# Optimization experiments

Hardware: AMD Instinct MI355X
Metric: run time of the kernel (lower is better)

## Reference

```python
import jax, jax.numpy as jnp
import numpy as np

MAX_SPAN_WIDTH = 12
THRESHOLD = 0.5


def _span_table(num_words):
    starts, ends = [], []
    for s in range(num_words):
        for e in range(s, min(num_words, s + MAX_SPAN_WIDTH)):
            starts.append(s)
            ends.append(e)
    return np.asarray(starts, np.int32), np.asarray(ends, np.int32)


def _mlp(x, w1, b1, w2, b2):
    # Linear -> LeakyReLU(0.01) -> Linear
    return jax.nn.leaky_relu(x @ w1 + b1, negative_slope=0.01) @ w2 + b2


def setup_inputs() -> dict:
    B, L, H, E, W, DFF = 8, 1024, 768, 16, 504, 512
    key = jax.random.key(0)
    ks = jax.random.split(key, 9)
    hidden_states = jax.random.normal(ks[0], (B, L, H), dtype=jnp.float32)
    # layout: first E tokens are entity-type tokens, next 2*W tokens are text (2 subwords/word)
    ent_mask = np.zeros((B, L), np.int32); ent_mask[:, :E] = 1
    text_mask = np.zeros((B, L), np.int32); text_mask[:, E:E + 2 * W] = 1
    word_index = np.full((B, L), -1, np.int32)
    word_index[:, E:E + 2 * W] = np.repeat(np.arange(W, dtype=np.int32), 2)[None, :]
    s = 0.02
    return {
        "hidden_states": hidden_states,
        "ent_w1": jax.random.normal(ks[1], (H, DFF), jnp.float32) * s,
        "ent_b1": jnp.zeros((DFF,), jnp.float32),
        "ent_w2": jax.random.normal(ks[2], (DFF, H), jnp.float32) * s,
        "ent_b2": jnp.zeros((H,), jnp.float32),
        "span_w1": jax.random.normal(ks[3], (2 * H, DFF), jnp.float32) * s,
        "span_b1": jnp.zeros((DFF,), jnp.float32),
        "span_w2": jax.random.normal(ks[4], (DFF, H), jnp.float32) * s,
        "span_b2": jnp.zeros((H,), jnp.float32),
        "text_mask": jnp.asarray(text_mask),
        "ent_mask": jnp.asarray(ent_mask),
        "word_index": jnp.asarray(word_index),
        "num_words": W,
        "num_ent": E,
    }


def reference(hidden_states, ent_w1, ent_b1, ent_w2, ent_b2,
              span_w1, span_b1, span_w2, span_b2,
              text_mask, ent_mask, word_index, num_words, num_ent):
    B, L, H = hidden_states.shape
    W, E = int(num_words), int(num_ent)

    # ---- word-level mean pooling over subword tokens (WordTokenRepresentation) ----
    valid = (text_mask == 1) & (word_index >= 0)                       # [B,L]
    oh = ((word_index[..., None] == jnp.arange(W)) & valid[..., None]).astype(hidden_states.dtype)  # [B,L,W]
    counts = jnp.maximum(oh.sum(axis=1), 1.0)                          # [B,W]
    word_emb = jnp.einsum('blw,blh->bwh', oh, hidden_states) / counts[..., None]

    # ---- gather entity-type tokens in order (EntityTokenRepresentation) ----
    keyv = jnp.where(ent_mask == 1, jnp.arange(L), L + jnp.arange(L))
    ent_pos = jnp.argsort(keyv, axis=-1)[:, :E]                        # [B,E]
    ent_tok = jnp.take_along_axis(hidden_states, ent_pos[..., None], axis=1)  # [B,E,H]
    ent_vec = _mlp(ent_tok, ent_w1, ent_b1, ent_w2, ent_b2)            # [B,E,H]

    # ---- span representations (all spans of width < MAX_SPAN_WIDTH) ----
    starts_np, ends_np = _span_table(W)                                # [N]
    span_in = jnp.concatenate([word_emb[:, starts_np], word_emb[:, ends_np]], axis=-1)  # [B,N,2H]
    span_vec = _mlp(span_in, span_w1, span_b1, span_w2, span_b2)       # [B,N,H]

    # ---- matching logits ----
    logits = jnp.einsum('bnh,beh->bne', span_vec, ent_vec)             # [B,N,E]

    # ---- NMS-style greedy decode (flat mode): threshold + score sort + overlap rejection ----
    N = logits.shape[1]
    probs = jax.nn.sigmoid(logits).reshape(B, N * E)
    cstart = jnp.repeat(jnp.asarray(starts_np), E)                     # [N*E]
    cend = jnp.repeat(jnp.asarray(ends_np), E)
    order = jnp.argsort(-probs, axis=-1)                               # score-descending
    probs_s = jnp.take_along_axis(probs, order, axis=-1)
    s_s, e_s = cstart[order], cend[order]
    pos = jnp.arange(W)

    def decode_one(pr, ss, ee):
        def body(cov, x):
            p, s, e = x
            m = (pos >= s) & (pos <= e)                                # candidate span mask over words
            take = (p > THRESHOLD) & ~jnp.any(cov & m)                 # flat: reject any overlap
            return cov | (m & take), take
        _, taken = jax.lax.scan(body, jnp.zeros((W,), bool), (pr, ss, ee))
        return taken

    taken_sorted = jax.vmap(decode_one)(probs_s, s_s, e_s)             # [B,N*E]
    inv = jnp.argsort(order, axis=-1)
    selected = jnp.take_along_axis(taken_sorted, inv, axis=-1).reshape(B, N, E)
    return logits, selected
```

## Files before the change

kernel.cpp:

```cpp
#include <hip/hip_runtime.h>
#include <hip/hip_bf16.h>
#include <stdint.h>

#define B_ 8
#define L_ 1024
#define H_ 768
#define E_ 16
#define W_ 504
#define DFF_ 512
#define N_ 5982
#define NE_ (N_*E_)
#define BNE_ (B_*NE_)
#define MAXK48 0x0000FFFFFFFFFFFFull
#define PT6_ 6

typedef unsigned long long u64;
typedef unsigned int u32;

__device__ __forceinline__ int rowstart_of(int s){
    int s0 = W_ - 11;
    if (s <= s0) return 12*s;
    int t = s - s0;
    return 12*s0 + t*11 - (t*(t-1))/2;
}

__device__ __forceinline__ u64 shflup_u64(u64 x, int d){
    u32 lo = (u32)__shfl_up((int)(u32)x, d, 64);
    u32 hi = (u32)__shfl_up((int)(u32)(x >> 32), d, 64);
    return ((u64)hi << 32) | (u64)lo;
}
__device__ __forceinline__ u64 shflxor_u64(u64 x, int m){
    u32 lo = (u32)__shfl_xor((int)(u32)x, m, 64);
    u32 hi = (u32)__shfl_xor((int)(u32)(x >> 32), m, 64);
    return ((u64)hi << 32) | (u64)lo;
}

__global__ void k_prolog(const int* __restrict__ ent_mask, int* __restrict__ ent_pos,
                         int* __restrict__ starts, int* __restrict__ ends,
                         int* __restrict__ tokc){
    int blk = blockIdx.x; int tid = threadIdx.x;
    if (blk == 8){
        for (int s = tid; s < W_; s += 256){
            int rs = rowstart_of(s);
            int cnt = min(12, W_ - s);
            for (int i = 0; i < cnt; i++){ starts[rs+i] = s; ends[rs+i] = s+i; }
        }
        for (int i = tid; i < B_*W_; i += 256) tokc[i] = 0;
        return;
    }
    __shared__ u32 wt[4]; __shared__ u32 cbase;
    int b = blk;
    int lane = tid & 63, wave = tid >> 6;
    if (tid == 0) cbase = 0;
    __syncthreads();
    for (int base = 0; base < L_; base += 256){
        int l = base + tid;
        bool f = (ent_mask[b*L_ + l] == 1);
        u64 bal = __ballot(f);
        if (lane == 0) wt[wave] = (u32)__popcll(bal);
        __syncthreads();
        u32 pre = cbase;
        for (int w = 0; w < 4; w++) if (w < wave) pre += wt[w];
        if (f){
            u32 rank = pre + (u32)__popcll(bal & ((1ull<<lane)-1ull));
            if (rank < E_) ent_pos[b*E_ + rank] = l;
        }
        __syncthreads();
        if (tid == 0){ u32 r = cbase; for (int w = 0; w < 4; w++) r += wt[w]; cbase = r; }
        __syncthreads();
    }
    u32 totEnt = cbase;
    if (totEnt >= E_) return;
    for (int base = 0; base < L_; base += 256){
        int l = base + tid;
        bool f = (ent_mask[b*L_ + l] != 1);
        u64 bal = __ballot(f);
        if (lane == 0) wt[wave] = (u32)__popcll(bal);
        __syncthreads();
        u32 pre = cbase;
        for (int w = 0; w < 4; w++) if (w < wave) pre += wt[w];
        if (f){
            u32 rank = pre + (u32)__popcll(bal & ((1ull<<lane)-1ull));
            if (rank < E_) ent_pos[b*E_ + rank] = l;
        }
        __syncthreads();
        if (tid == 0){ u32 r = cbase; for (int w = 0; w < 4; w++) r += wt[w]; cbase = r; }
        __syncthreads();
    }
}

__global__ void k_toklist(const int* __restrict__ tm, const int* __restrict__ wi,
                          int* __restrict__ tok, int* __restrict__ tokc){
    int i = blockIdx.x*256 + threadIdx.x;
    if (i >= B_*L_) return;
    int w = wi[i];
    if (tm[i] == 1 && w >= 0 && w < W_){
        int b = i / L_;
        int bw = b*W_ + w;
        int pos = atomicAdd(&tokc[bw], 1);
        if (pos < 4) tok[bw*4 + pos] = i - b*L_;
    }
}

__global__ void k_poolsort(const float* __restrict__ hs, const int* __restrict__ tok,
                           const int* __restrict__ tokc, float* __restrict__ wemb){
    __shared__ int stok[4]; __shared__ int scnt;
    int bw = blockIdx.x;
    int b = bw / W_;
    int tid = threadIdx.x;
    if (tid == 0){
        int c = tokc[bw]; int cc = min(c, 4);
        int v[4];
        for (int k = 0; k < cc; k++) v[k] = tok[bw*4 + k];
        for (int a = 1; a < cc; a++){ int x = v[a]; int j = a-1; while (j >= 0 && v[j] > x){ v[j+1] = v[j]; j--; } v[j+1] = x; }
        for (int k = 0; k < cc; k++) stok[k] = v[k];
        scnt = c;
    }
    __syncthreads();
    int c = scnt; int cc = min(c, 4);
    float denom = (float)max(c, 1);
    for (int h = tid; h < H_; h += 256){
        double s = 0.0;
        for (int k = 0; k < cc; k++)
            s += (double)hs[((size_t)(b*L_ + stok[k]))*H_ + h];
        wemb[(size_t)bw*H_ + h] = (float)(s / (double)denom);
    }
}

__global__ void k_ent1(const float* __restrict__ hs, const int* __restrict__ ent_pos,
                       const float* __restrict__ w1, const float* __restrict__ b1,
                       float* __restrict__ hidg){
    __shared__ float x[H_];
    int blk = blockIdx.x;
    int be = blk >> 1; int half = blk & 1;
    int b = be >> 4;
    int tid = threadIdx.x;
    int pos = ent_pos[be];
    const float* xp = hs + ((size_t)b*L_ + pos)*H_;
    for (int j = tid; j < H_; j += 256) x[j] = xp[j];
    __syncthreads();
    int d = half*256 + tid;
    float a0=0.f,a1=0.f,a2=0.f,a3=0.f;
    const float* wp = w1 + d;
    #pragma unroll 8
    for (int h = 0; h < H_; h += 4){
        a0 += x[h+0]*wp[(size_t)(h+0)*DFF_];
        a1 += x[h+1]*wp[(size_t)(h+1)*DFF_];
        a2 += x[h+2]*wp[(size_t)(h+2)*DFF_];
        a3 += x[h+3]*wp[(size_t)(h+3)*DFF_];
    }
    float acc = ((a0+a1)+(a2+a3)) + b1[d];
    hidg[(size_t)be*DFF_ + d] = acc > 0.f ? acc : 0.01f*acc;
}

__global__ void k_ent2(const float* __restrict__ hidg,
                       const float* __restrict__ w2, const float* __restrict__ b2,
                       float* __restrict__ ent_vec){
    __shared__ float hsd[DFF_];
    int blk = blockIdx.x;
    int be = blk / 3; int third = blk % 3;
    int tid = threadIdx.x;
    const float* hp = hidg + (size_t)be*DFF_;
    for (int j = tid; j < DFF_; j += 256) hsd[j] = hp[j];
    __syncthreads();
    int j = third*256 + tid;
    float a0=0.f,a1=0.f,a2=0.f,a3=0.f;
    const float* wp = w2 + j;
    #pragma unroll 8
    for (int d = 0; d < DFF_; d += 4){
        a0 += hsd[d+0]*wp[(size_t)(d+0)*H_];
        a1 += hsd[d+1]*wp[(size_t)(d+1)*H_];
        a2 += hsd[d+2]*wp[(size_t)(d+2)*H_];
        a3 += hsd[d+3]*wp[(size_t)(d+3)*H_];
    }
    ent_vec[(size_t)be*H_ + j] = ((a0+a1)+(a2+a3)) + b2[j];
}

__global__ void k_Mc(const float* __restrict__ span_w2, const float* __restrict__ span_b2,
                     const float* __restrict__ ent_vec, float* __restrict__ M,
                     float* __restrict__ cvec){
    int blk = blockIdx.x;
    if (blk == 256){
        int i = threadIdx.x;
        if (i < B_*E_){
            const float* ev = ent_vec + (size_t)i*H_;
            double acc = 0.0;
            for (int h = 0; h < H_; h++) acc += (double)span_b2[h]*(double)ev[h];
            cvec[i] = (float)acc;
        }
        return;
    }
    int b = blk/32; int dbase = (blk%32)*16;
    int tid = threadIdx.x; int d = dbase + (tid>>4); int e = tid&15;
    const float* ev = ent_vec + ((size_t)b*E_ + e)*H_;
    const float* wr = span_w2 + (size_t)d*H_;
    double p0=0.0, p1=0.0;
    for (int h = 0; h < H_; h += 2){
        p0 += (double)wr[h]*(double)ev[h];
        p1 += (double)wr[h+1]*(double)ev[h+1];
    }
    M[((size_t)b*DFF_ + d)*E_ + e] = (float)(p0+p1);
}

__global__ void k_pq(const float* __restrict__ wemb, const float* __restrict__ w1,
                     float* __restrict__ PQ, int b0){
    __shared__ float As[16][68];
    __shared__ float Bs[16][68];
    int bx = blockIdx.x & 15;
    int by = blockIdx.x >> 4;
    int tid = threadIdx.x;
    int tm = tid >> 4, tn = tid & 15;
    const float* A0 = wemb + (size_t)b0*W_*H_;
    int colbase = bx*64;
    const float* Bbase = (colbase < DFF_) ? w1 : (w1 + (size_t)H_*DFF_);
    int bcol0 = (colbase < DFF_) ? colbase : (colbase - DFF_);
    float acc[4][4] = {{0.f}};
    int ar = tid >> 2, akq = tid & 3;
    int bkk = tid >> 4, bcq = tid & 15;
    const int ROWS = 4*W_;
    for (int k0 = 0; k0 < H_; k0 += 16){
        {
            int gr = by*64 + ar;
            float4 av;
            if (gr < ROWS) av = *(const float4*)(A0 + (size_t)gr*H_ + k0 + akq*4);
            else av = make_float4(0.f,0.f,0.f,0.f);
            As[akq*4+0][ar] = av.x; As[akq*4+1][ar] = av.y;
            As[akq*4+2][ar] = av.z; As[akq*4+3][ar] = av.w;
        }
        {
            float4 bv = *(const float4*)(Bbase + (size_t)(k0+bkk)*DFF_ + bcol0 + bcq*4);
            Bs[bkk][bcq*4+0] = bv.x; Bs[bkk][bcq*4+1] = bv.y;
            Bs[bkk][bcq*4+2] = bv.z; Bs[bkk][bcq*4+3] = bv.w;
        }
        __syncthreads();
        #pragma unroll
        for (int kk = 0; kk < 16; kk++){
            float4 a = *(const float4*)&As[kk][tm*4];
            float4 bv = *(const float4*)&Bs[kk][tn*4];
            acc[0][0] += a.x*bv.x; acc[0][1] += a.x*bv.y; acc[0][2] += a.x*bv.z; acc[0][3] += a.x*bv.w;
            acc[1][0] += a.y*bv.x; acc[1][1] += a.y*bv.y; acc[1][2] += a.y*bv.z; acc[1][3] += a.y*bv.w;
            acc[2][0] += a.z*bv.x; acc[2][1] += a.z*bv.y; acc[2][2] += a.z*bv.z; acc[2][3] += a.z*bv.w;
            acc[3][0] += a.w*bv.x; acc[3][1] += a.w*bv.y; acc[3][2] += a.w*bv.z; acc[3][3] += a.w*bv.w;
        }
        __syncthreads();
    }
    #pragma unroll
    for (int r = 0; r < 4; r++){
        int gr = by*64 + tm*4 + r;
        if (gr < ROWS){
            float4 ov = make_float4(acc[r][0], acc[r][1], acc[r][2], acc[r][3]);
            *(float4*)(PQ + (size_t)gr*1024 + colbase + tn*4) = ov;
        }
    }
}

__global__ void k_logits(const float* __restrict__ PQ, const float* __restrict__ Mmat,
                         const float* __restrict__ cvec, const float* __restrict__ span_b1,
                         float* __restrict__ logits, float* __restrict__ outL, int b0){
    __shared__ float Ps[DFF_];
    __shared__ float hid[DFF_];
    __shared__ double redw[64];
    __shared__ float csh[E_];
    int blk = blockIdx.x;
    int bl = blk / W_; int s = blk - bl*W_;
    int b = b0 + bl;
    int tid = threadIdx.x;
    int lane = tid & 63, wave = tid >> 6;
    int ee = tid & 15; int g = tid >> 4;
    float Mreg[32];
    {
        const float* Mp = Mmat + (size_t)b*DFF_*E_ + (size_t)(g*32)*E_ + ee;
        #pragma unroll
        for (int i = 0; i < 32; i++) Mreg[i] = Mp[(size_t)i*E_];
    }
    const float* P = PQ + ((size_t)(bl*W_ + s))*1024;
    for (int d = tid; d < DFF_; d += 256) Ps[d] = P[d] + span_b1[d];
    if (tid < E_) csh[tid] = cvec[b*E_ + tid];
    __syncthreads();
    int nsp = min(12, W_ - s);
    int nbase = rowstart_of(s);
    for (int i = 0; i < nsp; i++){
        int e = s + i;
        const float* Q = PQ + ((size_t)(bl*W_ + e))*1024 + DFF_;
        for (int d = tid; d < DFF_; d += 256){
            float h = Ps[d] + Q[d];
            hid[d] = h > 0.f ? h : 0.01f*h;
        }
        __syncthreads();
        {
            int d0 = g*32;
            double a0=0.0, a1=0.0, a2=0.0, a3=0.0;
            #pragma unroll
            for (int k = 0; k < 32; k += 4){
                a0 += (double)hid[d0+k+0]*(double)Mreg[k+0];
                a1 += (double)hid[d0+k+1]*(double)Mreg[k+1];
                a2 += (double)hid[d0+k+2]*(double)Mreg[k+2];
                a3 += (double)hid[d0+k+3]*(double)Mreg[k+3];
            }
            double acc = (a0+a1)+(a2+a3);
            double t = acc + __shfl_down(acc, 32, 64);
            t = t + __shfl_down(t, 16, 64);
            if (lane < 16) redw[wave*16 + lane] = t;
        }
        __syncthreads();
        if (tid < E_){
            double t = ((redw[tid] + redw[16+tid]) + (redw[32+tid] + redw[48+tid]))
                     + (double)csh[tid];
            float lg = (float)t;
            size_t oi = ((size_t)b*N_ + nbase + i)*E_ + tid;
            logits[oi] = lg;
            outL[oi] = lg;
        }
        __syncthreads();
    }
}

__global__ void k_spanbest(const float* __restrict__ logits,
                           const int* __restrict__ starts, const int* __restrict__ ends,
                           u64* __restrict__ candS, float* __restrict__ outSel){
    int idx = blockIdx.x*256 + threadIdx.x;
    if (idx >= B_*N_) return;
    int b = idx / N_; int n = idx - b*N_;
    const float* lg = logits + (size_t)b*NE_ + (size_t)n*16;
    u64 best = ~0ull;
    for (int e = 0; e < 16; e++){
        float prob = 1.0f/(1.0f + expf(-lg[e]));
        if (prob > 0.5f){
            u32 key24 = (~__float_as_uint(prob)) & 0xFFFFFFu;
            u64 pk = ((u64)key24 << 24) | (u64)(u32)(n*16 + e);
            best = best < pk ? best : pk;
        }
    }
    int s = starts[n], e2 = ends[n];
    int len = e2 - s + 1;
    u64 packed = best;
    if (best != ~0ull)
        packed = best | ((u64)(u32)s << 48) | ((u64)(u32)(len-1) << 57);
    candS[idx] = packed;
    float* selp = outSel + (size_t)BNE_ + (size_t)b*NE_ + (size_t)n*16;
    float4 z = make_float4(0.f,0.f,0.f,0.f);
    *(float4*)(selp+0)  = z; *(float4*)(selp+4)  = z;
    *(float4*)(selp+8)  = z; *(float4*)(selp+12) = z;
}

__device__ __forceinline__ void decode_wave(const u64* sp, int n,
                                            float* __restrict__ outSel, int b){
    int lane = threadIdx.x & 63;
    u64 scov[8];
    #pragma unroll
    for (int k = 0; k < 8; k++) scov[k] = 0ull;
    int covcnt = 0;
    for (int base = 0; base < n; base += 64){
        int i = base + lane;
        bool has = i < n;
        u64 v = has ? sp[i] : ~0ull;
        int s   = (int)((v >> 48) & 0x1FFull);
        int len = (int)((v >> 57) & 0xFull) + 1;
        u32 c   = (u32)(v & 0xFFFFFFull);
        int w0 = s >> 6, sh0 = s & 63;
        int w1i = (w0 < 7) ? w0 + 1 : 7;
        u64 full = (1ull << len) - 1ull;
        u64 m0 = has ? (full << sh0) : 0ull;
        u64 m1 = (has && sh0 + len > 64) ? (full >> (64 - sh0)) : 0ull;
        u64 myc0 = 0ull, myc1 = 0ull;
        #pragma unroll
        for (int k = 0; k < 8; k++){
            if (w0  == k) myc0 = scov[k];
            if (w1i == k) myc1 = scov[k];
        }
        bool alive = has && (((myc0 & m0) | (myc1 & m1)) == 0ull);
        bool accept = false;
        u64 balv = __ballot(alive);
        if (balv){
            u64 pm[8];
            #pragma unroll
            for (int k = 0; k < 8; k++){
                u64 t = 0ull;
                if (alive){
                    if (w0  == k) t |= m0;
                    if (w1i == k) t |= m1;
                }
                pm[k] = t;
            }
            #pragma unroll
            for (int st = 1; st < 64; st <<= 1){
                #pragma unroll
                for (int k = 0; k < 8; k++) pm[k] |= shflup_u64(pm[k], st);
            }
            u64 ex0 = 0ull, ex1 = 0ull;
            #pragma unroll
            for (int k = 0; k < 8; k++){
                u64 e = shflup_u64(pm[k], 1);
                e = (lane == 0) ? 0ull : e;
                if (w0  == k) ex0 = e;
                if (w1i == k) ex1 = e;
            }
            bool blocked = (((ex0 & m0) | (ex1 & m1)) != 0ull);
            bool newacc = alive && !blocked;
            accept = newacc;
            u64 am[8];
            #pragma unroll
            for (int k = 0; k < 8; k++){
                u64 t = 0ull;
                if (newacc){
                    if (w0  == k) t |= m0;
                    if (w1i == k) t |= m1;
                }
                am[k] = t;
            }
            #pragma unroll
            for (int st = 1; st < 64; st <<= 1){
                #pragma unroll
                for (int k = 0; k < 8; k++) am[k] |= shflxor_u64(am[k], st);
            }
            #pragma unroll
            for (int k = 0; k < 8; k++){
                covcnt += (int)__popcll(am[k]);
                scov[k] |= am[k];
            }
            u64 pend = __ballot(alive && blocked);
            u32 vlo = (u32)v, vhi = (u32)(v >> 32);
            u64 accm = 0ull;
            while (pend){
                int j = (int)__builtin_ctzll(pend);
                pend &= pend - 1ull;
#if __has_builtin(__builtin_amdgcn_readlane)
                u32 jlo = (u32)__builtin_amdgcn_readlane((int)vlo, j);
                u32 jhi = (u32)__builtin_amdgcn_readlane((int)vhi, j);
#else
                u32 jlo = (u32)__shfl((int)vlo, j, 64);
                u32 jhi = (u32)__shfl((int)vhi, j, 64);
#endif
                u64 jv = ((u64)jhi << 32) | (u64)jlo;
                int js   = (int)((jv >> 48) & 0x1FFull);
                int jlen = (int)((jv >> 57) & 0xFull) + 1;
                int jw0 = js >> 6, jsh = js & 63;
                int jw1 = (jw0 < 7) ? jw0 + 1 : 7;
                u64 jfull = (1ull << jlen) - 1ull;
                u64 jm0 = jfull << jsh;
                u64 jm1 = (jsh + jlen > 64) ? (jfull >> (64 - jsh)) : 0ull;
                u64 c0 = 0ull, c1 = 0ull;
                #pragma unroll
                for (int k = 0; k < 8; k++){
                    if (jw0 == k) c0 = scov[k];
                    if (jw1 == k) c1 = scov[k];
                }
                bool ok = (((c0 & jm0) | (c1 & jm1)) == 0ull);
                u64 okm = ok ? ~0ull : 0ull;
                #pragma unroll
                for (int k = 0; k < 8; k++){
                    u64 add = 0ull;
                    if (jw0 == k) add |= jm0;
                    if (jw1 == k) add |= jm1;
                    scov[k] |= (add & okm);
                }
                covcnt += ok ? jlen : 0;
                accm |= (okm & (1ull << j));
            }
            if (((accm >> lane) & 1ull) != 0ull) accept = true;
        }
        if (accept)
            outSel[(size_t)BNE_ + (size_t)b*NE_ + (size_t)c] = 1.0f;
        if (covcnt >= W_) break;
    }
}

__global__ __launch_bounds__(1024) void k_tail(const u64* __restrict__ candS,
                                               float* __restrict__ outSel){
    __shared__ u64 cs[6032];
    __shared__ u64 Ma[512], Mb[512];
    __shared__ u32 wtot[16];
    __shared__ int nsh;
    int b = blockIdx.x; int tid = threadIdx.x;
    int lane = tid & 63, wave = tid >> 6;
    const u64* cSg = candS + (size_t)b*N_;

    #pragma unroll
    for (int k = 0; k < 5; k++) cs[tid + k*1024] = cSg[tid + k*1024];
    { int i5 = tid + 5*1024; if (i5 < N_) cs[i5] = cSg[i5]; }
    __syncthreads();

    if (tid < 512) Ma[tid] = (tid < W_) ? (cs[rowstart_of(tid)] & MAXK48) : MAXK48;
    __syncthreads();
    u64* Mcur = Ma; u64* Mnext = Mb;
    for (int l = 2; l <= 12; l++){
        if (tid < 512){
            int s = tid;
            u64 key = MAXK48; int idx = -1;
            if (s + l <= W_){ idx = rowstart_of(s) + (l-1); key = cs[idx] & MAXK48; }
            u64 a = Mcur[s];
            u64 bb = (s + 1 < 512) ? Mcur[s+1] : MAXK48;
            u64 dom = a < bb ? a : bb;
            if (idx >= 0 && dom < key) cs[idx] = ~0ull;
            Mnext[s] = dom < key ? dom : key;
        }
        __syncthreads();
        u64* t = Mcur; Mcur = Mnext; Mnext = t;
    }

    {
        int base = tid*PT6_;
        u64 vv[PT6_];
        u32 flags = 0; int cnt = 0;
        #pragma unroll
        for (int k = 0; k < PT6_; k++){
            int i = base + k;
            u64 v = (i < N_) ? cs[i] : ~0ull;
            vv[k] = v;
            if (v != ~0ull){ flags |= (1u << k); cnt++; }
        }
        u32 inc = (u32)cnt;
        for (int d = 1; d < 64; d <<= 1){ u32 o = (u32)__shfl_up((int)inc, d, 64); if (lane >= d) inc += o; }
        if (lane == 63) wtot[wave] = inc;
        __syncthreads();
        u32 woffs = 0;
        for (int w = 0; w < 16; w++) if (w < wave) woffs += wtot[w];
        u32 off = woffs + inc - (u32)cnt;
        if (tid == 1023) nsh = (int)(woffs + inc);
        #pragma unroll
        for (int k = 0; k < PT6_; k++){
            if (flags & (1u << k)) cs[off++] = vv[k];
        }
    }
    __syncthreads();
    int n = nsh;
    if (tid < 32) cs[n + tid] = ~0ull;
    __syncthreads();

    if (n <= 2048){
        u64 v0=~0ull, v1=~0ull;
        u64 k0=0, k1=0;
        if (tid        < n){ v0 = cs[tid];        k0 = v0 & MAXK48; }
        if (tid + 1024 < n){ v1 = cs[tid + 1024]; k1 = v1 & MAXK48; }
        u32 r0=0, r1=0;
        for (int j = 0; j < n; j += 16){
            u64 c[16];
            #pragma unroll
            for (int q = 0; q < 16; q++) c[q] = cs[j+q] & MAXK48;
            #pragma unroll
            for (int q = 0; q < 16; q++){
                r0 += (u32)(c[q] < k0);
                r1 += (u32)(c[q] < k1);
            }
        }
        __syncthreads();
        if (tid        < n) cs[r0] = v0;
        if (tid + 1024 < n) cs[r1] = v1;
        __syncthreads();
    } else {
        u64 vv[PT6_]; u32 rr[PT6_];
        #pragma unroll
        for (int k = 0; k < PT6_; k++){ vv[k] = ~0ull; rr[k] = 0; }
        #pragma unroll
        for (int k = 0; k < PT6_; k++){
            int i = tid + (k << 10);
            if (i < n){
                u64 v = cs[i];
                vv[k] = v;
                u64 ki = v & MAXK48;
                u32 r = 0;
                for (int j = 0; j < n; j += 8){
                    u64 c0 = cs[j+0]&MAXK48, c1 = cs[j+1]&MAXK48;
                    u64 c2 = cs[j+2]&MAXK48, c3 = cs[j+3]&MAXK48;
                    u64 c4 = cs[j+4]&MAXK48, c5 = cs[j+5]&MAXK48;
                    u64 c6 = cs[j+6]&MAXK48, c7 = cs[j+7]&MAXK48;
                    r += (u32)(c0<ki) + (u32)(c1<ki) + (u32)(c2<ki) + (u32)(c3<ki)
                       + (u32)(c4<ki) + (u32)(c5<ki) + (u32)(c6<ki) + (u32)(c7<ki);
                }
                rr[k] = r;
            }
        }
        __syncthreads();
        #pragma unroll
        for (int k = 0; k < PT6_; k++){
            int i = tid + (k << 10);
            if (i < n) cs[rr[k]] = vv[k];
        }
        __syncthreads();
    }

    if (wave == 0) decode_wave(cs, n, outSel, b);
}

extern "C" void kernel_launch(void* const* d_in, const int* in_sizes, int n_in,
                              void* d_out, int out_size, void* d_ws, size_t ws_size,
                              hipStream_t stream){
    const float* hs        = (const float*)d_in[0];
    const float* ent_w1    = (const float*)d_in[1];
    const float* ent_b1    = (const float*)d_in[2];
    const float* ent_w2    = (const float*)d_in[3];
    const float* ent_b2    = (const float*)d_in[4];
    const float* span_w1   = (const float*)d_in[5];
    const float* span_b1   = (const float*)d_in[6];
    const float* span_w2   = (const float*)d_in[7];
    const float* span_b2   = (const float*)d_in[8];
    const int*  text_mask  = (const int*)d_in[9];
    const int*  ent_mask   = (const int*)d_in[10];
    const int*  word_index = (const int*)d_in[11];
    float* out = (float*)d_out;

    char* wsbase = (char*)d_ws; size_t off = 0;
    auto alloc = [&](size_t bytes)->void*{ void* p = wsbase + off; off = (off + bytes + 255) & ~(size_t)255; return p; };
    char*  region1 = (char*)alloc((size_t)B_*W_*H_*4);
    float* wemb   = (float*)region1;
    u64*   candS  = (u64*)region1;
    int*   tok    = (int*)  alloc((size_t)B_*W_*4*4);
    int*   tokc   = (int*)  alloc((size_t)B_*W_*4);
    float* PQ     = (float*)alloc((size_t)4*W_*1024*4);
    float* logits = (float*)alloc((size_t)BNE_*4);
    int*   entpos = (int*)  alloc((size_t)B_*E_*4);
    float* hidg   = (float*)alloc((size_t)B_*E_*DFF_*4);
    float* entvec = (float*)alloc((size_t)B_*E_*H_*4);
    float* Mmat   = (float*)alloc((size_t)B_*DFF_*E_*4);
    float* cvec   = (float*)alloc((size_t)B_*E_*4);
    int*   starts = (int*)  alloc((size_t)N_*4);
    int*   ends   = (int*)  alloc((size_t)N_*4);

    k_prolog<<<9,256,0,stream>>>(ent_mask, entpos, starts, ends, tokc);
    k_toklist<<<(B_*L_+255)/256,256,0,stream>>>(text_mask, word_index, tok, tokc);
    k_poolsort<<<B_*W_,256,0,stream>>>(hs, tok, tokc, wemb);
    k_ent1<<<B_*E_*2,256,0,stream>>>(hs, entpos, ent_w1, ent_b1, hidg);
    k_ent2<<<B_*E_*3,256,0,stream>>>(hidg, ent_w2, ent_b2, entvec);
    k_Mc<<<257,256,0,stream>>>(span_w2, span_b2, entvec, Mmat, cvec);
    for (int b0 = 0; b0 < B_; b0 += 4){
        k_pq<<<512,256,0,stream>>>(wemb, span_w1, PQ, b0);
        k_logits<<<4*W_,256,0,stream>>>(PQ, Mmat, cvec, span_b1, logits, out, b0);
    }
    k_spanbest<<<(B_*N_+255)/256,256,0,stream>>>(logits, starts, ends, candS, out);
    k_tail<<<B_,1024,0,stream>>>(candS, out);
}
```

Before: 440.9 us.

## Replace sort-first decode with parallel local-max greedy rounds and double-buffer GEMM loads

The tail kernel no longer runs a domination prune followed by a full rank sort of all candidates. It builds a (length, start) key table and repeatedly accepts spans whose key is the minimum over every word they cover, then kills overlapping spans. Only once few candidates remain does it sort them and hand them to the serial wave decode, seeded with the coverage found so far. Separately, the k_pq GEMM now uses a 32-wide k tile with register prefetch of the next tile, to cut barriers and hide load latency. The tail block shrinks to 256 threads, and the iterative rounds could run many times on adversarial inputs.

After: 468.7 us. 1.06x slower.

```diff
diff --git a/kernel.cpp b/kernel.cpp
--- a/kernel.cpp
+++ b/kernel.cpp
@@ -12,7 +12,7 @@
 #define NE_ (N_*E_)
 #define BNE_ (B_*NE_)
 #define MAXK48 0x0000FFFFFFFFFFFFull
-#define PT6_ 6
+#define PT_ 24
 
 typedef unsigned long long u64;
 typedef unsigned int u32;
@@ -204,8 +204,8 @@
 
 __global__ void k_pq(const float* __restrict__ wemb, const float* __restrict__ w1,
                      float* __restrict__ PQ, int b0){
-    __shared__ float As[16][68];
-    __shared__ float Bs[16][68];
+    __shared__ float As[32][68];
+    __shared__ float Bs[32][68];
     int bx = blockIdx.x & 15;
     int by = blockIdx.x >> 4;
     int tid = threadIdx.x;
@@ -218,23 +218,34 @@
     int ar = tid >> 2, akq = tid & 3;
     int bkk = tid >> 4, bcq = tid & 15;
     const int ROWS = 4*W_;
-    for (int k0 = 0; k0 < H_; k0 += 16){
-        {
-            int gr = by*64 + ar;
-            float4 av;
-            if (gr < ROWS) av = *(const float4*)(A0 + (size_t)gr*H_ + k0 + akq*4);
-            else av = make_float4(0.f,0.f,0.f,0.f);
-            As[akq*4+0][ar] = av.x; As[akq*4+1][ar] = av.y;
-            As[akq*4+2][ar] = av.z; As[akq*4+3][ar] = av.w;
-        }
-        {
-            float4 bv = *(const float4*)(Bbase + (size_t)(k0+bkk)*DFF_ + bcol0 + bcq*4);
-            Bs[bkk][bcq*4+0] = bv.x; Bs[bkk][bcq*4+1] = bv.y;
-            Bs[bkk][bcq*4+2] = bv.z; Bs[bkk][bcq*4+3] = bv.w;
-        }
-        __syncthreads();
+    int gr = by*64 + ar;
+    bool aok = (gr < ROWS);
+    const float* Ap = A0 + (size_t)gr*H_ + akq*4;
+    const float* Bp = Bbase + (size_t)bkk*DFF_ + bcol0 + bcq*4;
+    float4 av0, av1, bv0, bv1;
+    av0 = aok ? *(const float4*)(Ap + 0)  : make_float4(0.f,0.f,0.f,0.f);
+    av1 = aok ? *(const float4*)(Ap + 16) : make_float4(0.f,0.f,0.f,0.f);
+    bv0 = *(const float4*)(Bp + 0);
+    bv1 = *(const float4*)(Bp + (size_t)16*DFF_);
+    for (int k0 = 0; k0 < H_; k0 += 32){
+        As[akq*4+0][ar] = av0.x; As[akq*4+1][ar] = av0.y;
+        As[akq*4+2][ar] = av0.z; As[akq*4+3][ar] = av0.w;
+        As[16+akq*4+0][ar] = av1.x; As[16+akq*4+1][ar] = av1.y;
+        As[16+akq*4+2][ar] = av1.z; As[16+akq*4+3][ar] = av1.w;
+        Bs[bkk][bcq*4+0] = bv0.x; Bs[bkk][bcq*4+1] = bv0.y;
+        Bs[bkk][bcq*4+2] = bv0.z; Bs[bkk][bcq*4+3] = bv0.w;
+        Bs[16+bkk][bcq*4+0] = bv1.x; Bs[16+bkk][bcq*4+1] = bv1.y;
+        Bs[16+bkk][bcq*4+2] = bv1.z; Bs[16+bkk][bcq*4+3] = bv1.w;
+        __syncthreads();
+        if (k0 + 32 < H_){
+            int kn = k0 + 32;
+            av0 = aok ? *(const float4*)(Ap + kn)      : make_float4(0.f,0.f,0.f,0.f);
+            av1 = aok ? *(const float4*)(Ap + kn + 16) : make_float4(0.f,0.f,0.f,0.f);
+            bv0 = *(const float4*)(Bp + (size_t)kn*DFF_);
+            bv1 = *(const float4*)(Bp + (size_t)(kn+16)*DFF_);
+        }
         #pragma unroll
-        for (int kk = 0; kk < 16; kk++){
+        for (int kk = 0; kk < 32; kk++){
             float4 a = *(const float4*)&As[kk][tm*4];
             float4 bv = *(const float4*)&Bs[kk][tn*4];
             acc[0][0] += a.x*bv.x; acc[0][1] += a.x*bv.y; acc[0][2] += a.x*bv.z; acc[0][3] += a.x*bv.w;
@@ -246,10 +257,10 @@
     }
     #pragma unroll
     for (int r = 0; r < 4; r++){
-        int gr = by*64 + tm*4 + r;
-        if (gr < ROWS){
+        int grr = by*64 + tm*4 + r;
+        if (grr < ROWS){
             float4 ov = make_float4(acc[r][0], acc[r][1], acc[r][2], acc[r][3]);
-            *(float4*)(PQ + (size_t)gr*1024 + colbase + tn*4) = ov;
+            *(float4*)(PQ + (size_t)grr*1024 + colbase + tn*4) = ov;
         }
     }
 }
@@ -343,13 +354,9 @@
     *(float4*)(selp+8)  = z; *(float4*)(selp+12) = z;
 }
 
-__device__ __forceinline__ void decode_wave(const u64* sp, int n,
-                                            float* __restrict__ outSel, int b){
+__device__ __forceinline__ void decode_wave_seeded(const u64* sp, int n, u64* scov,
+                                                   int covcnt, float* __restrict__ outSel, int b){
     int lane = threadIdx.x & 63;
-    u64 scov[8];
-    #pragma unroll
-    for (int k = 0; k < 8; k++) scov[k] = 0ull;
-    int covcnt = 0;
     for (int base = 0; base < n; base += 64){
         int i = base + lane;
         bool has = i < n;
@@ -465,78 +472,139 @@
     }
 }
 
-__global__ __launch_bounds__(1024) void k_tail(const u64* __restrict__ candS,
-                                               float* __restrict__ outSel){
-    __shared__ u64 cs[6032];
-    __shared__ u64 Ma[512], Mb[512];
-    __shared__ u32 wtot[16];
+__global__ __launch_bounds__(256) void k_tail(const u64* __restrict__ candS,
+                                              float* __restrict__ outSel){
+    __shared__ u64 kT[6160];
+    __shared__ u64 mcov[512];
+    __shared__ u32 cov[512];
+    __shared__ u32 wtot[4];
     __shared__ int nsh;
+    __shared__ int acnt;
     int b = blockIdx.x; int tid = threadIdx.x;
     int lane = tid & 63, wave = tid >> 6;
     const u64* cSg = candS + (size_t)b*N_;
 
     #pragma unroll
-    for (int k = 0; k < 5; k++) cs[tid + k*1024] = cSg[tid + k*1024];
-    { int i5 = tid + 5*1024; if (i5 < N_) cs[i5] = cSg[i5]; }
-    __syncthreads();
-
-    if (tid < 512) Ma[tid] = (tid < W_) ? (cs[rowstart_of(tid)] & MAXK48) : MAXK48;
-    __syncthreads();
-    u64* Mcur = Ma; u64* Mnext = Mb;
-    for (int l = 2; l <= 12; l++){
-        if (tid < 512){
-            int s = tid;
-            u64 key = MAXK48; int idx = -1;
-            if (s + l <= W_){ idx = rowstart_of(s) + (l-1); key = cs[idx] & MAXK48; }
-            u64 a = Mcur[s];
-            u64 bb = (s + 1 < 512) ? Mcur[s+1] : MAXK48;
-            u64 dom = a < bb ? a : bb;
-            if (idx >= 0 && dom < key) cs[idx] = ~0ull;
-            Mnext[s] = dom < key ? dom : key;
-        }
-        __syncthreads();
-        u64* t = Mcur; Mcur = Mnext; Mnext = t;
-    }
+    for (int k = 0; k < PT_; k++) kT[tid + (k<<8)] = MAXK48;
+    if (tid < 16) kT[6144 + tid] = MAXK48;
+    cov[tid] = 0u; cov[tid+256] = 0u;
+    __syncthreads();
+    #pragma unroll
+    for (int k = 0; k < PT_; k++){
+        int i = tid + (k<<8);
+        u64 v = (i < N_) ? cSg[i] : ~0ull;
+        if (v != ~0ull){
+            int s   = (int)((v >> 48) & 0x1FF);
+            int lm1 = (int)((v >> 57) & 0xF);
+            kT[(lm1<<9) + s] = v & MAXK48;
+        }
+    }
+    __syncthreads();
+    u32 alive = 0;
+    #pragma unroll
+    for (int k = 0; k < PT_; k++)
+        if (kT[tid + (k<<8)] != MAXK48) alive |= (1u << k);
+
+    while (true){
+        #pragma unroll
+        for (int q = 0; q < 2; q++){
+            int w = tid + (q<<8);
+            if (w < W_){
+                u64 m = MAXK48;
+                int dmax = min(11, w);
+                for (int d = 0; d <= dmax; d++){
+                    int s = w - d;
+                    int lmax = min(12, W_ - s);
+                    for (int l = d + 1; l <= lmax; l++){
+                        u64 kk = kT[((l-1)<<9) + s];
+                        if (kk < m) m = kk;
+                    }
+                }
+                mcov[w] = m;
+            }
+        }
+        __syncthreads();
+        u32 accm = 0;
+        u32 am = alive;
+        while (am){
+            int k = __builtin_ctz(am); am &= am - 1u;
+            int j = tid + (k<<8);
+            u64 key = kT[j];
+            int s = j & 511, len = (j >> 9) + 1;
+            u64 rmin = MAXK48;
+            for (int w = s; w < s + len; w++){ u64 t = mcov[w]; if (t < rmin) rmin = t; }
+            if (rmin == key){
+                accm |= (1u << k);
+                for (int w = s; w < s + len; w++) cov[w] = 1u;
+                u32 c = (u32)(key & 0xFFFFFFull);
+                outSel[(size_t)BNE_ + (size_t)b*NE_ + (size_t)c] = 1.0f;
+                kT[j] = MAXK48;
+            }
+        }
+        alive &= ~accm;
+        if (tid == 0) acnt = 0;
+        __syncthreads();
+        u32 killm = 0;
+        am = alive;
+        while (am){
+            int k = __builtin_ctz(am); am &= am - 1u;
+            int j = tid + (k<<8);
+            int s = j & 511, len = (j >> 9) + 1;
+            u32 f = 0;
+            for (int w = s; w < s + len; w++) f |= cov[w];
+            if (f){ killm |= (1u << k); kT[j] = MAXK48; }
+        }
+        alive &= ~killm;
+        atomicAdd(&acnt, (int)__popc(alive));
+        __syncthreads();
+        if (acnt <= 384) break;
+    }
+    int n_total = acnt;
 
     {
-        int base = tid*PT6_;
-        u64 vv[PT6_];
+        u64 vv[PT_];
         u32 flags = 0; int cnt = 0;
         #pragma unroll
-        for (int k = 0; k < PT6_; k++){
-            int i = base + k;
-            u64 v = (i < N_) ? cs[i] : ~0ull;
-            vv[k] = v;
-            if (v != ~0ull){ flags |= (1u << k); cnt++; }
+        for (int k = 0; k < PT_; k++){
+            int j = tid + (k<<8);
+            u64 key = kT[j];
+            u64 rec = ~0ull;
+            if ((alive >> k) & 1u){
+                int s = j & 511, lm1 = j >> 9;
+                rec = key | ((u64)(u32)s << 48) | ((u64)(u32)lm1 << 57);
+                flags |= (1u << k); cnt++;
+            }
+            vv[k] = rec;
         }
         u32 inc = (u32)cnt;
         for (int d = 1; d < 64; d <<= 1){ u32 o = (u32)__shfl_up((int)inc, d, 64); if (lane >= d) inc += o; }
         if (lane == 63) wtot[wave] = inc;
         __syncthreads();
         u32 woffs = 0;
-        for (int w = 0; w < 16; w++) if (w < wave) woffs += wtot[w];
+        for (int w = 0; w < 4; w++) if (w < wave) woffs += wtot[w];
         u32 off = woffs + inc - (u32)cnt;
-        if (tid == 1023) nsh = (int)(woffs + inc);
+        if (tid == 255) nsh = (int)(woffs + inc);
         #pragma unroll
-        for (int k = 0; k < PT6_; k++){
-            if (flags & (1u << k)) cs[off++] = vv[k];
+        for (int k = 0; k < PT_; k++){
+            if (flags & (1u << k)) kT[off++] = vv[k];
         }
     }
     __syncthreads();
     int n = nsh;
-    if (tid < 32) cs[n + tid] = ~0ull;
-    __syncthreads();
-
-    if (n <= 2048){
-        u64 v0=~0ull, v1=~0ull;
-        u64 k0=0, k1=0;
-        if (tid        < n){ v0 = cs[tid];        k0 = v0 & MAXK48; }
-        if (tid + 1024 < n){ v1 = cs[tid + 1024]; k1 = v1 & MAXK48; }
-        u32 r0=0, r1=0;
+    if (tid < 16) kT[n + tid] = ~0ull;
+    __syncthreads();
+    if (n == 0) return;
+
+    {
+        u64 v0 = ~0ull, v1 = ~0ull;
+        u64 k0 = 0, k1 = 0;
+        if (tid       < n){ v0 = kT[tid];       k0 = v0 & MAXK48; }
+        if (tid + 256 < n){ v1 = kT[tid + 256]; k1 = v1 & MAXK48; }
+        u32 r0 = 0, r1 = 0;
         for (int j = 0; j < n; j += 16){
             u64 c[16];
             #pragma unroll
-            for (int q = 0; q < 16; q++) c[q] = cs[j+q] & MAXK48;
+            for (int q = 0; q < 16; q++) c[q] = kT[j+q] & MAXK48;
             #pragma unroll
             for (int q = 0; q < 16; q++){
                 r0 += (u32)(c[q] < k0);
@@ -544,42 +612,23 @@
             }
         }
         __syncthreads();
-        if (tid        < n) cs[r0] = v0;
-        if (tid + 1024 < n) cs[r1] = v1;
-        __syncthreads();
-    } else {
-        u64 vv[PT6_]; u32 rr[PT6_];
+        if (tid       < n) kT[r0] = v0;
+        if (tid + 256 < n) kT[r1] = v1;
+        __syncthreads();
+    }
+
+    if (wave == 0){
+        u64 scov[8];
+        int covcnt = 0;
         #pragma unroll
-        for (int k = 0; k < PT6_; k++){ vv[k] = ~0ull; rr[k] = 0; }
-        #pragma unroll
-        for (int k = 0; k < PT6_; k++){
-            int i = tid + (k << 10);
-            if (i < n){
-                u64 v = cs[i];
-                vv[k] = v;
-                u64 ki = v & MAXK48;
-                u32 r = 0;
-                for (int j = 0; j < n; j += 8){
-                    u64 c0 = cs[j+0]&MAXK48, c1 = cs[j+1]&MAXK48;
-                    u64 c2 = cs[j+2]&MAXK48, c3 = cs[j+3]&MAXK48;
-                    u64 c4 = cs[j+4]&MAXK48, c5 = cs[j+5]&MAXK48;
-                    u64 c6 = cs[j+6]&MAXK48, c7 = cs[j+7]&MAXK48;
-                    r += (u32)(c0<ki) + (u32)(c1<ki) + (u32)(c2<ki) + (u32)(c3<ki)
-                       + (u32)(c4<ki) + (u32)(c5<ki) + (u32)(c6<ki) + (u32)(c7<ki);
-                }
-                rr[k] = r;
-            }
-        }
-        __syncthreads();
-        #pragma unroll
-        for (int k = 0; k < PT6_; k++){
-            int i = tid + (k << 10);
-            if (i < n) cs[rr[k]] = vv[k];
-        }
-        __syncthreads();
-    }
-
-    if (wave == 0) decode_wave(cs, n, outSel, b);
+        for (int k = 0; k < 8; k++){
+            u64 m = __ballot(cov[(k<<6) + lane] != 0u);
+            scov[k] = m;
+            covcnt += (int)__popcll(m);
+        }
+        decode_wave_seeded(kT, n, scov, covcnt, outSel, b);
+    }
+    (void)n_total;
 }
 
 extern "C" void kernel_launch(void* const* d_in, const int* in_sizes, int n_in,
@@ -627,5 +676,5 @@
         k_logits<<<4*W_,256,0,stream>>>(PQ, Mmat, cvec, span_b1, logits, out, b0);
     }
     k_spanbest<<<(B_*N_+255)/256,256,0,stream>>>(logits, starts, ends, candS, out);
-    k_tail<<<B_,1024,0,stream>>>(candS, out);
-}
+    k_tail<<<B_,256,0,stream>>>(candS, out);
+}
```
